# Optimization experiments

Measured on AMD Instinct MI355X. Metric: run time of the kernel, lower is better.

The kernel has to match this reference:

```python
import jax, jax.numpy as jnp
import numpy as np

ALPHA = 0.5
BETA = 0.5
N_CLASS = 128
EPS = 1e-9


def setup_inputs() -> dict:
    key = jax.random.key(0)
    k1, k2 = jax.random.split(key)
    y_pred = jax.random.normal(k1, (262144, N_CLASS), dtype=jnp.float32)
    y_true = jax.random.randint(k2, (262144,), 0, N_CLASS, dtype=jnp.int64)
    return {"y_pred": y_pred, "y_true": y_true}


def reference(y_pred, y_true):
    N = y_pred.shape[0]
    # Cross-entropy (mean reduction, as nn.CrossEntropyLoss default)
    logp = jax.nn.log_softmax(y_pred, axis=1)
    ce = -jnp.mean(jnp.take_along_axis(logp, y_true[:, None], axis=1))

    # Penalty term uses detached probabilities (y_pred.detach() in torch)
    p = jax.nn.softmax(jax.lax.stop_gradient(y_pred), axis=1)
    p1 = p[:, 0]  # probability of class 0 per sample

    # num_labels: class histogram (torch loop -> vectorized scatter-add)
    num_labels = jnp.zeros((N_CLASS,), dtype=y_pred.dtype).at[y_true].add(1.0)
    # sj(j) = beta * (1 - n_j / (sum(n) - n_0)), defined for j >= 1
    s = BETA * (1.0 - num_labels / (jnp.sum(num_labels) - num_labels[0]))

    # per-sample penalty: alpha*log(p1+eps) if label==0 else s[label]*log(1-p1+eps)
    per_sample = jnp.where(
        y_true == 0,
        ALPHA * jnp.log(p1 + EPS),
        s[y_true] * jnp.log(1.0 - p1 + EPS),
    )
    penalty = jnp.sum(per_sample)
    return ce - penalty / N
```

## Files before the change

kernel.cpp:

```cpp
#include <hip/hip_runtime.h>
#include <math.h>
#include <stdint.h>

#define NCLS 128
#define NBANK 8
constexpr float ALPHA = 0.5f;
constexpr float BETA_ = 0.5f;
constexpr float EPS_ = 1e-9f;

__global__ void zero_ws(uint32_t* __restrict__ ws) {
    const int t = threadIdx.x;
    for (int i = t; i < 3088; i += 256) ws[i] = 0u;
}

__global__ __launch_bounds__(1024, 4) void loss_main(
    const float* __restrict__ y_pred,
    const int*   __restrict__ y_true,
    double* __restrict__ gLb, unsigned int* __restrict__ gcntb,
    double* __restrict__ gceb, int nrows)
{
    __shared__ float    sL[NCLS];
    __shared__ unsigned scnt[NCLS];
    __shared__ float    sce;

    const int t = threadIdx.x;
    if (t == 0) sce = 0.f;
    if (t < NCLS) { sL[t] = 0.f; scnt[t] = 0u; }
    __syncthreads();

    const int lane = t & 63;
    const int half = lane >> 5;
    const int l32  = lane & 31;
    const int wgl  = blockIdx.x * (blockDim.x >> 6) + (t >> 6);
    const int nW   = gridDim.x * (blockDim.x >> 6);
    const int nPairs = nrows >> 1;

    float ce_local = 0.f;

    int p0 = wgl * 8;
    for (; p0 + 7 < nPairs; p0 += nW * 8) {
        float4 v[8]; int lab[8];
        const float* base = y_pred + ((size_t)(p0 << 1) + half) * NCLS + (l32 << 2);
        #pragma unroll
        for (int u = 0; u < 8; ++u) {
            v[u]   = *reinterpret_cast<const float4*>(base + (size_t)(u << 1) * NCLS);
            lab[u] = y_true[((p0 + u) << 1) + half];
        }
        float S[8];
        #pragma unroll
        for (int u = 0; u < 8; ++u) {
            const float ex = __expf(v[u].x), ey = __expf(v[u].y);
            const float ez = __expf(v[u].z), ew = __expf(v[u].w);
            S[u] = (ex + ey) + (ez + ew);
        }
        #pragma unroll
        for (int off = 16; off; off >>= 1) {
            #pragma unroll
            for (int u = 0; u < 8; ++u) S[u] += __shfl_xor(S[u], off);
        }
        float tv[8];
        #pragma unroll
        for (int u = 0; u < 8; ++u) {
            const int ls = lab[u] & 3;
            const float vsel = (ls == 0) ? v[u].x : (ls == 1) ? v[u].y
                             : (ls == 2) ? v[u].z : v[u].w;
            tv[u] = __shfl(vsel, (half << 5) + (lab[u] >> 2));
        }
        if (l32 == 0) {
            #pragma unroll
            for (int u = 0; u < 8; ++u) {
                ce_local += tv[u] - __logf(S[u]);
                const float p1 = __expf(v[u].x) / S[u];
                const float contrib = (lab[u] == 0) ? ALPHA * __logf(p1 + EPS_)
                                                    : __logf(1.f - p1 + EPS_);
                atomicAdd(&sL[lab[u]], contrib);
                atomicAdd(&scnt[lab[u]], 1u);
            }
        }
    }
    for (; p0 < nPairs; ++p0) {
        const int row = (p0 << 1) + half;
        const float4 v = *reinterpret_cast<const float4*>(
            y_pred + (size_t)row * NCLS + (l32 << 2));
        const int lab = y_true[row];
        const float ex = __expf(v.x), ey = __expf(v.y);
        const float ez = __expf(v.z), ew = __expf(v.w);
        float S = (ex + ey) + (ez + ew);
        #pragma unroll
        for (int off = 16; off; off >>= 1) S += __shfl_xor(S, off);
        const int ls = lab & 3;
        const float vsel = (ls == 0) ? v.x : (ls == 1) ? v.y : (ls == 2) ? v.z : v.w;
        const float tv = __shfl(vsel, (half << 5) + (lab >> 2));
        if (l32 == 0) {
            ce_local += tv - __logf(S);
            const float p1 = ex / S;
            const float contrib = (lab == 0) ? ALPHA * __logf(p1 + EPS_)
                                             : __logf(1.f - p1 + EPS_);
            atomicAdd(&sL[lab], contrib);
            atomicAdd(&scnt[lab], 1u);
        }
    }
    if (nrows & 1) {
        if (wgl == 0) {
            const int row = nrows - 1;
            const float4 v = *reinterpret_cast<const float4*>(
                y_pred + (size_t)row * NCLS + (l32 << 2));
            const int lab = y_true[row];
            const float ex = __expf(v.x), ey = __expf(v.y);
            const float ez = __expf(v.z), ew = __expf(v.w);
            float S = (ex + ey) + (ez + ew);
            #pragma unroll
            for (int off = 16; off; off >>= 1) S += __shfl_xor(S, off);
            const int ls = lab & 3;
            const float vsel = (ls == 0) ? v.x : (ls == 1) ? v.y : (ls == 2) ? v.z : v.w;
            const float tv = __shfl(vsel, (half << 5) + (lab >> 2));
            if (lane == 0) {
                ce_local += tv - __logf(S);
                const float p1 = ex / S;
                const float contrib = (lab == 0) ? ALPHA * __logf(p1 + EPS_)
                                                 : __logf(1.f - p1 + EPS_);
                atomicAdd(&sL[lab], contrib);
                atomicAdd(&scnt[lab], 1u);
            }
        }
    }

    float lp = ce_local;
    #pragma unroll
    for (int off = 32; off; off >>= 1) lp += __shfl_xor(lp, off);
    if (lane == 0) atomicAdd(&sce, lp);
    __syncthreads();

    const int bank = blockIdx.x & (NBANK - 1);
    if (t < NCLS) {
        const int c = (t + blockIdx.x) & (NCLS - 1);
        if (scnt[c]) {
            atomicAdd(&gLb[c * NBANK + bank], (double)sL[c]);
            atomicAdd(&gcntb[c * NBANK + bank], scnt[c]);
        }
    }
    if (t == 0) atomicAdd(&gceb[bank], (double)sce);
}

__global__ void loss_final(const double* __restrict__ gLb,
                           const unsigned int* __restrict__ gcntb,
                           const double* __restrict__ gceb,
                           float* __restrict__ out, int nrows)
{
    const int lane = threadIdx.x;
    double cnt0 = 0.0;
    #pragma unroll
    for (int b = 0; b < NBANK; ++b) cnt0 += (double)gcntb[0 * NBANK + b];
    const double denom = (double)nrows - cnt0;

    double local = 0.0;
    for (int c = lane; c < NCLS; c += 64) {
        double Lc = 0.0, nc = 0.0;
        #pragma unroll
        for (int b = 0; b < NBANK; ++b) {
            Lc += gLb[c * NBANK + b];
            nc += (double)gcntb[c * NBANK + b];
        }
        if (c == 0) local += Lc;
        else        local += (double)BETA_ * (1.0 - nc / denom) * Lc;
    }
    #pragma unroll
    for (int off = 32; off; off >>= 1) local += __shfl_down(local, off);
    if (lane == 0) {
        double ce = 0.0;
        #pragma unroll
        for (int b = 0; b < NBANK; ++b) ce += gceb[b];
        ce = -ce / (double)nrows;
        out[0] = (float)(ce - local / (double)nrows);
    }
}

extern "C" void kernel_launch(void* const* d_in, const int* in_sizes, int n_in,
                              void* d_out, int out_size, void* d_ws, size_t ws_size,
                              hipStream_t stream) {
    const float* y_pred = (const float*)d_in[0];
    const int*   y_true = (const int*)d_in[1];
    const int nrows = in_sizes[1];

    double*   gLb   = (double*)d_ws;
    double*   gceb  = (double*)((char*)d_ws + 8192);
    unsigned* gcntb = (unsigned*)((char*)d_ws + 8256);

    zero_ws<<<dim3(1), dim3(256), 0, stream>>>((uint32_t*)d_ws);

    loss_main<<<dim3(256), dim3(1024), 0, stream>>>(y_pred, y_true, gLb, gcntb, gceb, nrows);
    loss_final<<<dim3(1), dim3(64), 0, stream>>>(gLb, gcntb, gceb, (float*)d_out, nrows);
}
```

Measured before the change: 40.53 us.

## Double-buffer row loads in loss kernel and relaunch with 512x512 grid

Restructures the main loop as a two-buffer software pipeline: each iteration issues the next batch of eight row-pair loads before reducing the current batch. This is meant to hide global memory latency behind the exp and shuffle work. The launch moves from 256 blocks of 1024 threads to 512 blocks of 512, with launch bounds relaxed to (512, 2) so registers can hold both buffers. The tail loop gains a break guard and the odd-row path is reorganised. The extra register pressure may cut occupancy.

```diff
diff --git a/kernel.cpp b/kernel.cpp
--- a/kernel.cpp
+++ b/kernel.cpp
@@ -13,7 +13,7 @@
     for (int i = t; i < 3088; i += 256) ws[i] = 0u;
 }
 
-__global__ __launch_bounds__(1024, 4) void loss_main(
+__global__ __launch_bounds__(512, 2) void loss_main(
     const float* __restrict__ y_pred,
     const int*   __restrict__ y_true,
     double* __restrict__ gLb, unsigned int* __restrict__ gcntb,
@@ -34,25 +34,33 @@
     const int wgl  = blockIdx.x * (blockDim.x >> 6) + (t >> 6);
     const int nW   = gridDim.x * (blockDim.x >> 6);
     const int nPairs = nrows >> 1;
+    const int step = nW * 8;
 
     float ce_local = 0.f;
 
-    int p0 = wgl * 8;
-    for (; p0 + 7 < nPairs; p0 += nW * 8) {
-        float4 v[8]; int lab[8];
-        const float* base = y_pred + ((size_t)(p0 << 1) + half) * NCLS + (l32 << 2);
+    auto LOAD = [&](float4 (&V)[8], int (&L)[8], int pb) {
+        const float* base = y_pred + ((size_t)(pb << 1) + half) * NCLS + (l32 << 2);
         #pragma unroll
         for (int u = 0; u < 8; ++u) {
-            v[u]   = *reinterpret_cast<const float4*>(base + (size_t)(u << 1) * NCLS);
-            lab[u] = y_true[((p0 + u) << 1) + half];
-        }
-        float S[8];
+            V[u] = *reinterpret_cast<const float4*>(base + (size_t)(u << 1) * NCLS);
+            L[u] = y_true[((pb + u) << 1) + half];
+        }
+    };
+    auto EXP = [&](const float4 (&V)[8], const int (&L)[8],
+                   float (&S)[8], float (&vs)[8], float (&e0)[8]) {
         #pragma unroll
         for (int u = 0; u < 8; ++u) {
-            const float ex = __expf(v[u].x), ey = __expf(v[u].y);
-            const float ez = __expf(v[u].z), ew = __expf(v[u].w);
-            S[u] = (ex + ey) + (ez + ew);
-        }
+            const float ex = __expf(V[u].x), ey = __expf(V[u].y);
+            const float ez = __expf(V[u].z), ew = __expf(V[u].w);
+            e0[u] = ex;
+            S[u]  = (ex + ey) + (ez + ew);
+            const int ls = L[u] & 3;
+            vs[u] = (ls == 0) ? V[u].x : (ls == 1) ? V[u].y
+                  : (ls == 2) ? V[u].z : V[u].w;
+        }
+    };
+    auto REDU = [&](float (&S)[8], const float (&vs)[8], const float (&e0)[8],
+                    const int (&L)[8]) {
         #pragma unroll
         for (int off = 16; off; off >>= 1) {
             #pragma unroll
@@ -60,26 +68,55 @@
         }
         float tv[8];
         #pragma unroll
-        for (int u = 0; u < 8; ++u) {
-            const int ls = lab[u] & 3;
-            const float vsel = (ls == 0) ? v[u].x : (ls == 1) ? v[u].y
-                             : (ls == 2) ? v[u].z : v[u].w;
-            tv[u] = __shfl(vsel, (half << 5) + (lab[u] >> 2));
-        }
+        for (int u = 0; u < 8; ++u)
+            tv[u] = __shfl(vs[u], (half << 5) + (L[u] >> 2));
         if (l32 == 0) {
             #pragma unroll
             for (int u = 0; u < 8; ++u) {
                 ce_local += tv[u] - __logf(S[u]);
-                const float p1 = __expf(v[u].x) / S[u];
-                const float contrib = (lab[u] == 0) ? ALPHA * __logf(p1 + EPS_)
-                                                    : __logf(1.f - p1 + EPS_);
-                atomicAdd(&sL[lab[u]], contrib);
-                atomicAdd(&scnt[lab[u]], 1u);
-            }
-        }
-    }
-    for (; p0 < nPairs; ++p0) {
-        const int row = (p0 << 1) + half;
+                const float p1 = e0[u] / S[u];
+                const float contrib = (L[u] == 0) ? ALPHA * __logf(p1 + EPS_)
+                                                  : __logf(1.f - p1 + EPS_);
+                atomicAdd(&sL[L[u]], contrib);
+                atomicAdd(&scnt[L[u]], 1u);
+            }
+        }
+    };
+
+    int p = wgl * 8;
+    if (p + 7 < nPairs) {
+        float4 VA[8], VB[8]; int LA[8], LB[8];
+        float SA[8], vsA[8], e0A[8], SB[8], vsB[8], e0B[8];
+        LOAD(VA, LA, p);
+        int pn = p + step;
+        bool hn = (pn + 7 < nPairs);
+        if (hn) LOAD(VB, LB, pn);
+        while (true) {
+            EXP(VA, LA, SA, vsA, e0A);
+            {
+                const int p2 = pn + step;
+                if (hn && p2 + 7 < nPairs) LOAD(VA, LA, p2);
+            }
+            REDU(SA, vsA, e0A, LA);
+            p = pn;
+            if (!hn) break;
+            pn = p + step;
+            hn = (pn + 7 < nPairs);
+            EXP(VB, LB, SB, vsB, e0B);
+            {
+                const int p2 = pn + step;
+                if (hn && p2 + 7 < nPairs) LOAD(VB, LB, p2);
+            }
+            REDU(SB, vsB, e0B, LB);
+            p = pn;
+            if (!hn) break;
+            pn = p + step;
+            hn = (pn + 7 < nPairs);
+        }
+    }
+    for (; p < nPairs; p += 1) {
+        if (p < wgl * 8 || ((p - wgl * 8) % step) >= 8) break;
+        const int row = (p << 1) + half;
         const float4 v = *reinterpret_cast<const float4*>(
             y_pred + (size_t)row * NCLS + (l32 << 2));
         const int lab = y_true[row];
@@ -100,12 +137,12 @@
             atomicAdd(&scnt[lab], 1u);
         }
     }
-    if (nrows & 1) {
-        if (wgl == 0) {
-            const int row = nrows - 1;
-            const float4 v = *reinterpret_cast<const float4*>(
-                y_pred + (size_t)row * NCLS + (l32 << 2));
-            const int lab = y_true[row];
+    if ((nrows & 1) && wgl == 0) {
+        const int row = nrows - 1;
+        const float4 v = *reinterpret_cast<const float4*>(
+            y_pred + (size_t)row * NCLS + (l32 << 2));
+        const int lab = y_true[row];
+        if (half == 0) {
             const float ex = __expf(v.x), ey = __expf(v.y);
             const float ez = __expf(v.z), ew = __expf(v.w);
             float S = (ex + ey) + (ez + ew);
@@ -114,7 +151,7 @@
             const int ls = lab & 3;
             const float vsel = (ls == 0) ? v.x : (ls == 1) ? v.y : (ls == 2) ? v.z : v.w;
             const float tv = __shfl(vsel, (half << 5) + (lab >> 2));
-            if (lane == 0) {
+            if (l32 == 0) {
                 ce_local += tv - __logf(S);
                 const float p1 = ex / S;
                 const float contrib = (lab == 0) ? ALPHA * __logf(p1 + EPS_)
@@ -188,6 +225,6 @@
 
     zero_ws<<<dim3(1), dim3(256), 0, stream>>>((uint32_t*)d_ws);
 
-    loss_main<<<dim3(256), dim3(1024), 0, stream>>>(y_pred, y_true, gLb, gcntb, gceb, nrows);
+    loss_main<<<dim3(512), dim3(512), 0, stream>>>(y_pred, y_true, gLb, gcntb, gceb, nrows);
     loss_final<<<dim3(1), dim3(64), 0, stream>>>(gLb, gcntb, gceb, (float*)d_out, nrows);
 }
```

After: 53.01 us. 1.31x slower.
